# Performance work log

Hardware: AMD Instinct MI355X
Metric: run time of the kernel (lower is better)

The kernel has to match this reference:

```python
import jax, jax.numpy as jnp
import numpy as np

NUM_EXPERTS = 8
TOP_K = 2
INIT_STD = 0.02


def setup_inputs() -> dict:
    key = jax.random.key(0)
    ks = jax.random.split(key, 10)
    B, S, H, I, SI, E = 2, 512, 2048, 1408, 5632, NUM_EXPERTS
    return {
        "hidden_states": jax.random.normal(ks[0], (B, S, H), jnp.float32),
        "gate_w": jax.random.normal(ks[1], (H, E), jnp.float32) * INIT_STD,
        "w_gate": jax.random.normal(ks[2], (E, H, I), jnp.float32) * INIT_STD,
        "w_up": jax.random.normal(ks[3], (E, H, I), jnp.float32) * INIT_STD,
        "w_down": jax.random.normal(ks[4], (E, I, H), jnp.float32) * INIT_STD,
        "sw_gate": jax.random.normal(ks[5], (H, SI), jnp.float32) * INIT_STD,
        "sw_up": jax.random.normal(ks[6], (H, SI), jnp.float32) * INIT_STD,
        "sw_down": jax.random.normal(ks[7], (SI, H), jnp.float32) * INIT_STD,
        "shared_gate_w": jax.random.normal(ks[8], (H, 1), jnp.float32) * INIT_STD,
    }


def reference(hidden_states, gate_w, w_gate, w_up, w_down, sw_gate, sw_up, sw_down, shared_gate_w):
    # Router: logits [B,S,E] in float32, softmax, top-k (norm_topk_prob=False)
    router_logits = (hidden_states @ gate_w).astype(jnp.float32)
    routing_weights = jax.nn.softmax(router_logits, axis=-1)
    top_w, sel = jax.lax.top_k(routing_weights, TOP_K)  # [B,S,K]
    # Scatter top-k weights back to dense per-expert weights [B,S,E]
    # (equals sum_k (sel==e) * top_w, as in the original masked accumulation)
    w = (jax.nn.one_hot(sel, NUM_EXPERTS, dtype=top_w.dtype) * top_w[..., None]).sum(axis=-2)
    # Dense loop over all experts, vectorized as batched einsum (same math)
    g = jnp.einsum('bsh,ehi->bsei', hidden_states, w_gate)
    u = jnp.einsum('bsh,ehi->bsei', hidden_states, w_up)
    expert_out = jnp.einsum('bsei,eih->bseh', jax.nn.silu(g) * u, w_down)  # [B,S,E,H]
    moe_out = jnp.einsum('bse,bseh->bsh', w.astype(hidden_states.dtype), expert_out)
    # Shared expert with sigmoid gate
    shared = (jax.nn.silu(hidden_states @ sw_gate) * (hidden_states @ sw_up)) @ sw_down
    shared = jax.nn.sigmoid(hidden_states @ shared_gate_w) * shared
    return moe_out + shared, router_logits
```

## Files before the change

kernel.cpp:

```cpp
#include <hip/hip_runtime.h>
#include <hip/hip_bf16.h>

#define T_TOK 1024
#define HDIM  2048
#define NEXP  8
#define IDIM  1408
#define SIDIM 5632
#define MAXSLOTS 24

typedef __attribute__((ext_vector_type(8))) short bf16x8;
typedef __attribute__((ext_vector_type(4))) float f32x4;
typedef unsigned short ushort_t;

__device__ __forceinline__ unsigned f2bf(float x) {
    unsigned u = __float_as_uint(x);
    return (u + 0x7fffu + ((u >> 16) & 1u)) >> 16;
}
__device__ __forceinline__ unsigned pack2(float a, float b) {
    return f2bf(a) | (f2bf(b) << 16);
}
__device__ __forceinline__ void async16(const void* g, void* l) {
    __builtin_amdgcn_global_load_lds(
        (const __attribute__((address_space(1))) void*)g,
        (__attribute__((address_space(3))) void*)l, 16, 0, 0);
}

#define PIPE_BAR()    __builtin_amdgcn_s_barrier()
#define SCHED_FENCE() __builtin_amdgcn_sched_barrier(0)
#define WAIT_VM8()    asm volatile("s_waitcnt vmcnt(8)" ::: "memory")
#define WAIT_VM0()    asm volatile("s_waitcnt vmcnt(0)" ::: "memory")

__global__ __launch_bounds__(256) void conv_x(
    const float* __restrict__ src, ushort_t* __restrict__ dst)
{
    const int i = blockIdx.x * 256 + threadIdx.x;
    const float4* s = (const float4*)src + (size_t)i * 2;
    float4 a = s[0], b = s[1];
    union { ushort_t us[8]; uint4 v; } o;
    o.us[0] = (ushort_t)f2bf(a.x); o.us[1] = (ushort_t)f2bf(a.y);
    o.us[2] = (ushort_t)f2bf(a.z); o.us[3] = (ushort_t)f2bf(a.w);
    o.us[4] = (ushort_t)f2bf(b.x); o.us[5] = (ushort_t)f2bf(b.y);
    o.us[6] = (ushort_t)f2bf(b.z); o.us[7] = (ushort_t)f2bf(b.w);
    ((uint4*)dst)[i] = o.v;
}

__global__ __launch_bounds__(256) void conv_all(
    const float* __restrict__ wg, const float* __restrict__ wu,
    const float* __restrict__ wd, const float* __restrict__ swg,
    const float* __restrict__ swu, const float* __restrict__ swd,
    ushort_t* __restrict__ wtg, ushort_t* __restrict__ wtu,
    ushort_t* __restrict__ wtd, ushort_t* __restrict__ swtg,
    ushort_t* __restrict__ swtu, ushort_t* __restrict__ swtd)
{
    int id = blockIdx.x;
    const float* src; ushort_t* dst; int K, N, ktile, ntile;
    if (id < 11264) {
        const float* s0; ushort_t* d0;
        if (id < 5632) { s0 = wg; d0 = wtg; } else { s0 = wu; d0 = wtu; id -= 5632; }
        const int e = id / 704, t = id % 704;
        K = 2048; N = 1408;
        src = s0 + (size_t)e * K * N; dst = d0 + (size_t)e * K * N;
        ntile = t % 22; ktile = t / 22;
    } else if (id < 16896) {
        const int t2 = id - 11264;
        const int e = t2 / 704, t = t2 % 704;
        K = 1408; N = 2048;
        src = wd + (size_t)e * K * N; dst = wtd + (size_t)e * K * N;
        ntile = t % 32; ktile = t / 32;
    } else if (id < 22528) {
        int t2 = id - 16896; const float* s0; ushort_t* d0;
        if (t2 < 2816) { s0 = swg; d0 = swtg; } else { s0 = swu; d0 = swtu; t2 -= 2816; }
        K = 2048; N = 5632;
        src = s0; dst = d0;
        ntile = t2 % 88; ktile = t2 / 88;
    } else {
        const int t2 = id - 22528;
        K = 5632; N = 2048; src = swd; dst = swtd;
        ntile = t2 % 32; ktile = t2 / 32;
    }
    const int tid = threadIdx.x;
    __shared__ __align__(16) unsigned ldsw[32 * 68];
    const float* sp = src + (size_t)(ktile * 64) * N + ntile * 64;
    const int m = tid & 15;
    const int ph = tid >> 4;
#pragma unroll
    for (int h = 0; h < 2; ++h) {
        const int P = ph + h * 16;
        const float* r0 = sp + (size_t)(2 * P) * N + m * 4;
        f32x4 a = __builtin_nontemporal_load((const f32x4*)r0);
        f32x4 b = __builtin_nontemporal_load((const f32x4*)(r0 + N));
        uint4 u;
        u.x = pack2(a[0], b[0]); u.y = pack2(a[1], b[1]);
        u.z = pack2(a[2], b[2]); u.w = pack2(a[3], b[3]);
        *(uint4*)&ldsw[P * 68 + 4 * (m ^ (P >> 2))] = u;
    }
    __syncthreads();
    ushort_t* dp = dst + (size_t)(ntile * 64) * K + ktile * 64;
#pragma unroll
    for (int j = 0; j < 2; ++j) {
        const int c = tid + j * 256;
        const int row = c >> 3, kc = c & 7;
        const int base = 4 * ((row >> 2) ^ kc) + (row & 3);
        uint4 v;
        v.x = ldsw[(4 * kc + 0) * 68 + base];
        v.y = ldsw[(4 * kc + 1) * 68 + base];
        v.z = ldsw[(4 * kc + 2) * 68 + base];
        v.w = ldsw[(4 * kc + 3) * 68 + base];
        *(uint4*)(dp + (size_t)row * K + kc * 8) = v;
    }
}

__global__ __launch_bounds__(256) void router_kernel(
    const float* __restrict__ hs, const float* __restrict__ gw,
    const float* __restrict__ sgw, float* __restrict__ out_logits,
    float* __restrict__ w_dense, float* __restrict__ sgate,
    int* __restrict__ counts, int* __restrict__ tok_list)
{
    const int t = blockIdx.x;
    const int tid = threadIdx.x;
    const float* h = hs + (size_t)t * HDIM;
    float acc[9];
#pragma unroll
    for (int e = 0; e < 9; ++e) acc[e] = 0.f;
    for (int i = tid; i < HDIM; i += 256) {
        float hv = h[i];
        const float4* g4 = (const float4*)(gw + (size_t)i * NEXP);
        float4 g0 = g4[0], g1 = g4[1];
        acc[0] += hv * g0.x; acc[1] += hv * g0.y;
        acc[2] += hv * g0.z; acc[3] += hv * g0.w;
        acc[4] += hv * g1.x; acc[5] += hv * g1.y;
        acc[6] += hv * g1.z; acc[7] += hv * g1.w;
        acc[8] += hv * sgw[i];
    }
#pragma unroll
    for (int e = 0; e < 9; ++e)
        for (int off = 32; off > 0; off >>= 1)
            acc[e] += __shfl_down(acc[e], off, 64);
    __shared__ float lds[4][9];
    const int wid = tid >> 6, lane = tid & 63;
    if (lane == 0)
        for (int e = 0; e < 9; ++e) lds[wid][e] = acc[e];
    __syncthreads();
    if (tid == 0) {
        float l[9];
        for (int e = 0; e < 9; ++e)
            l[e] = lds[0][e] + lds[1][e] + lds[2][e] + lds[3][e];
        for (int e = 0; e < NEXP; ++e) out_logits[(size_t)t * NEXP + e] = l[e];
        float m = l[0];
        for (int e = 1; e < NEXP; ++e) m = fmaxf(m, l[e]);
        float p[NEXP], s = 0.f;
        for (int e = 0; e < NEXP; ++e) { p[e] = expf(l[e] - m); s += p[e]; }
        float inv = 1.f / s;
        for (int e = 0; e < NEXP; ++e) p[e] *= inv;
        int e0 = 0;
        for (int e = 1; e < NEXP; ++e) if (p[e] > p[e0]) e0 = e;
        int e1 = (e0 == 0) ? 1 : 0;
        for (int e = 0; e < NEXP; ++e) if (e != e0 && p[e] > p[e1]) e1 = e;
        for (int e = 0; e < NEXP; ++e)
            w_dense[(size_t)t * NEXP + e] = (e == e0) ? p[e0] : ((e == e1) ? p[e1] : 0.f);
        sgate[t] = 1.f / (1.f + expf(-l[8]));
        int p0 = atomicAdd(&counts[e0], 1); tok_list[e0 * T_TOK + p0] = t;
        int p1 = atomicAdd(&counts[e1], 1); tok_list[e1 * T_TOK + p1] = t;
    }
}

__global__ __launch_bounds__(64) void slot_kernel(
    const int* __restrict__ counts, int* __restrict__ slot_e,
    int* __restrict__ slot_rb, int* __restrict__ nslots)
{
    if (threadIdx.x == 0 && blockIdx.x == 0) {
        int ns = 0;
        for (int e = 0; e < NEXP; ++e)
            for (int b = 0; b < counts[e]; b += 128) {
                slot_e[ns] = e; slot_rb[ns] = b; ++ns;
            }
        nslots[0] = ns;
    }
}

__global__ __launch_bounds__(256) void gateup_all(
    const ushort_t* __restrict__ Xb,
    const ushort_t* __restrict__ swtg, const ushort_t* __restrict__ swtu,
    const ushort_t* __restrict__ wtg, const ushort_t* __restrict__ wtu,
    ushort_t* __restrict__ Ysh, ushort_t* __restrict__ Yr,
    const int* __restrict__ slot_e, const int* __restrict__ slot_rb,
    const int* __restrict__ counts, const int* __restrict__ nslots,
    const int* __restrict__ tok_list, const ushort_t* __restrict__ zerobuf)
{
    const int id = blockIdx.x;
    int n0, slot, e, rowbase, N, mode;
    if (id < 704) {
        mode = 1; n0 = (id % 88) * 64; slot = id / 88; e = 0; rowbase = 0; N = SIDIM;
    } else {
        mode = 0;
        const int id2 = id - 704;
        n0 = (id2 % 22) * 64; slot = id2 / 22;
        if (slot >= nslots[0]) return;
        e = slot_e[slot]; rowbase = slot_rb[slot]; N = IDIM;
    }
    const ushort_t* __restrict__ Wg = mode ? swtg : wtg + (size_t)e * HDIM * IDIM;
    const ushort_t* __restrict__ Wu = mode ? swtu : wtu + (size_t)e * HDIM * IDIM;
    ushort_t* __restrict__ Y = mode ? Ysh : Yr;
    const int K = HDIM;

    const int tid = threadIdx.x, lane = tid & 63, wid = tid >> 6;
    const int wr = (wid >> 1) * 64;
    const int wc = (wid & 1) * 32;
    const int fm = lane & 15, kg = lane >> 4;

    __shared__ int ltok[128];
    __shared__ __align__(16) ushort_t Xa[2][128 * 64];
    __shared__ __align__(16) ushort_t Bgs[2][64 * 64];
    __shared__ __align__(16) ushort_t Bus[2][64 * 64];

    if (tid < 128) {
        int tg;
        if (mode == 0) {
            int cnt = counts[e];
            tg = (rowbase + tid < cnt) ? tok_list[e * T_TOK + rowbase + tid] : -1;
        } else {
            tg = slot * 128 + tid;
        }
        ltok[tid] = tg;
    }
    __syncthreads();

    f32x4 ag[4][2], au[4][2];
#pragma unroll
    for (int a = 0; a < 4; ++a)
#pragma unroll
        for (int b = 0; b < 2; ++b) {
            ag[a][b] = f32x4{0.f, 0.f, 0.f, 0.f};
            au[a][b] = f32x4{0.f, 0.f, 0.f, 0.f};
        }

    const int koff = (((tid & 7) ^ ((tid >> 3) & 7))) * 8;
    const ushort_t* pA[4];
#pragma unroll
    for (int j = 0; j < 4; ++j) {
        const int r = (tid >> 3) + j * 32;
        const int tk = ltok[r];
        pA[j] = (tk >= 0) ? Xb + (size_t)tk * K + koff : zerobuf;
    }
    const ushort_t* pG[2];
    const ushort_t* pU[2];
#pragma unroll
    for (int j = 0; j < 2; ++j) {
        const int r = (tid >> 3) + j * 32;
        pG[j] = Wg + (size_t)(n0 + r) * K + koff;
        pU[j] = Wu + (size_t)(n0 + r) * K + koff;
    }

#define GU_STAGE(xp, gp, up, k0)                                            \
    {                                                                       \
        _Pragma("unroll")                                                   \
        for (int j = 0; j < 4; ++j)                                         \
            async16(pA[j] + (k0), &(xp)[(j * 256 + wid * 64) * 8]);         \
        _Pragma("unroll")                                                   \
        for (int j = 0; j < 2; ++j) {                                       \
            async16(pG[j] + (k0), &(gp)[(j * 256 + wid * 64) * 8]);         \
            async16(pU[j] + (k0), &(up)[(j * 256 + wid * 64) * 8]);         \
        }                                                                   \
    }

#define GU_COMP(xa, bg, bu)                                                 \
    {                                                                       \
        _Pragma("unroll")                                                   \
        for (int ks = 0; ks < 2; ++ks) {                                    \
            const int kx = ((ks * 4 + kg) ^ (fm & 7)) * 8;                  \
            bf16x8 af[4];                                                   \
            _Pragma("unroll")                                               \
            for (int mt = 0; mt < 4; ++mt)                                  \
                af[mt] = *(const bf16x8*)&(xa)[(wr + mt * 16 + fm) * 64 + kx]; \
            _Pragma("unroll")                                               \
            for (int nt = 0; nt < 2; ++nt) {                                \
                const int rb = (wc + nt * 16 + fm) * 64 + kx;               \
                bf16x8 bgv = *(const bf16x8*)&(bg)[rb];                     \
                bf16x8 buv = *(const bf16x8*)&(bu)[rb];                     \
                _Pragma("unroll")                                           \
                for (int mt = 0; mt < 4; ++mt) {                            \
                    ag[mt][nt] = __builtin_amdgcn_mfma_f32_16x16x32_bf16(af[mt], bgv, ag[mt][nt], 0, 0, 0); \
                    au[mt][nt] = __builtin_amdgcn_mfma_f32_16x16x32_bf16(af[mt], buv, au[mt][nt], 0, 0, 0); \
                }                                                           \
            }                                                               \
        }                                                                   \
    }

    const int NT = K / 64;
    GU_STAGE(Xa[0], Bgs[0], Bus[0], 0);
    GU_STAGE(Xa[1], Bgs[1], Bus[1], 64);

    int t = 0;
    for (; t + 3 < NT; t += 2) {
        WAIT_VM8(); PIPE_BAR(); SCHED_FENCE();
        GU_COMP(Xa[0], Bgs[0], Bus[0]);
        SCHED_FENCE(); PIPE_BAR(); SCHED_FENCE();
        GU_STAGE(Xa[0], Bgs[0], Bus[0], (t + 2) * 64);

        WAIT_VM8(); PIPE_BAR(); SCHED_FENCE();
        GU_COMP(Xa[1], Bgs[1], Bus[1]);
        SCHED_FENCE(); PIPE_BAR(); SCHED_FENCE();
        GU_STAGE(Xa[1], Bgs[1], Bus[1], (t + 3) * 64);
    }
    if (t + 2 < NT) {
        WAIT_VM8(); PIPE_BAR(); SCHED_FENCE();
        GU_COMP(Xa[0], Bgs[0], Bus[0]);
        SCHED_FENCE(); PIPE_BAR(); SCHED_FENCE();
        GU_STAGE(Xa[0], Bgs[0], Bus[0], (t + 2) * 64);
        WAIT_VM8(); PIPE_BAR(); SCHED_FENCE();
        GU_COMP(Xa[1], Bgs[1], Bus[1]);
        WAIT_VM0(); PIPE_BAR(); SCHED_FENCE();
        GU_COMP(Xa[0], Bgs[0], Bus[0]);
    } else {
        WAIT_VM8(); PIPE_BAR(); SCHED_FENCE();
        GU_COMP(Xa[0], Bgs[0], Bus[0]);
        WAIT_VM0(); PIPE_BAR(); SCHED_FENCE();
        GU_COMP(Xa[1], Bgs[1], Bus[1]);
    }
#undef GU_STAGE
#undef GU_COMP

#pragma unroll
    for (int mt = 0; mt < 4; ++mt)
#pragma unroll
        for (int nt = 0; nt < 2; ++nt) {
            const int col = n0 + wc + nt * 16 + fm;
#pragma unroll
            for (int i = 0; i < 4; ++i) {
                const int row = wr + mt * 16 + kg * 4 + i;
                float g = ag[mt][nt][i], u = au[mt][nt][i];
                float yv = g / (1.f + expf(-g)) * u;
                Y[(size_t)(slot * 128 + row) * N + col] = (ushort_t)f2bf(yv);
            }
        }
}

__global__ __launch_bounds__(256) void down_all(
    const ushort_t* __restrict__ Ysh, const ushort_t* __restrict__ Yr,
    const ushort_t* __restrict__ swtd, const ushort_t* __restrict__ wtd,
    float* __restrict__ out,
    const int* __restrict__ slot_e, const int* __restrict__ slot_rb,
    const int* __restrict__ counts, const int* __restrict__ nslots,
    const int* __restrict__ tok_list, const float* __restrict__ w_dense,
    const float* __restrict__ sgate)
{
    const int id = blockIdx.x;
    int n0, slot, e, rowbase, K, kbase, ksteps, mode;
    const ushort_t* Yb;
    const ushort_t* Wd;
    if (id < 512) {
        mode = 1;
        n0 = (id & 15) * 128; slot = (id >> 4) & 7;
        const int z = id >> 7;
        K = SIDIM; kbase = z * 1408; ksteps = 22;
        e = 0; rowbase = 0;
        Yb = Ysh + (size_t)slot * 128 * K;
        Wd = swtd;
    } else {
        mode = 0;
        const int id2 = id - 512;
        n0 = (id2 & 15) * 128;
        const int rest = id2 >> 4;
        slot = rest >> 1;
        if (slot >= nslots[0]) return;
        const int z = rest & 1;
        K = IDIM; kbase = z * 704; ksteps = 11;
        e = slot_e[slot]; rowbase = slot_rb[slot];
        Yb = Yr + (size_t)slot * 128 * K;
        Wd = wtd + (size_t)e * IDIM * HDIM;
    }
    const int tid = threadIdx.x, lane = tid & 63, wid = tid >> 6;
    const int wr = (wid >> 1) * 64;
    const int wc = (wid & 1) * 64;
    const int fm = lane & 15, kg = lane >> 4;

    __shared__ int ltok[128];
    __shared__ float lw[128];
    __shared__ __align__(16) ushort_t Ya[2][128 * 64];
    __shared__ __align__(16) ushort_t Bd[2][128 * 64];

    if (tid < 128) {
        int tg; float wv;
        if (mode == 0) {
            int cnt = counts[e];
            if (rowbase + tid < cnt) {
                tg = tok_list[e * T_TOK + rowbase + tid];
                wv = w_dense[(size_t)tg * NEXP + e];
            } else { tg = -1; wv = 0.f; }
        } else {
            tg = slot * 128 + tid; wv = sgate[tg];
        }
        ltok[tid] = tg; lw[tid] = wv;
    }
    __syncthreads();

    f32x4 acc[4][4];
#pragma unroll
    for (int a = 0; a < 4; ++a)
#pragma unroll
        for (int b = 0; b < 4; ++b) acc[a][b] = f32x4{0.f, 0.f, 0.f, 0.f};

    const int koff = (((tid & 7) ^ ((tid >> 3) & 7))) * 8;
    const ushort_t* pY[4];
    const ushort_t* pW[4];
#pragma unroll
    for (int j = 0; j < 4; ++j) {
        const int r = (tid >> 3) + j * 32;
        pY[j] = Yb + (size_t)r * K + kbase + koff;
        pW[j] = Wd + (size_t)(n0 + r) * K + kbase + koff;
    }

#define D_STAGE(yp, bp, k0)                                                 \
    {                                                                       \
        _Pragma("unroll")                                                   \
        for (int j = 0; j < 4; ++j) {                                       \
            async16(pY[j] + (k0), &(yp)[(j * 256 + wid * 64) * 8]);         \
            async16(pW[j] + (k0), &(bp)[(j * 256 + wid * 64) * 8]);         \
        }                                                                   \
    }

#define D_COMP(ya, bd)                                                      \
    {                                                                       \
        _Pragma("unroll")                                                   \
        for (int ks = 0; ks < 2; ++ks) {                                    \
            const int kx = ((ks * 4 + kg) ^ (fm & 7)) * 8;                  \
            bf16x8 af[4];                                                   \
            _Pragma("unroll")                                               \
            for (int mt = 0; mt < 4; ++mt)                                  \
                af[mt] = *(const bf16x8*)&(ya)[(wr + mt * 16 + fm) * 64 + kx]; \
            _Pragma("unroll")                                               \
            for (int nt = 0; nt < 4; ++nt) {                                \
                bf16x8 bfv = *(const bf16x8*)&(bd)[(wc + nt * 16 + fm) * 64 + kx]; \
                _Pragma("unroll")                                           \
                for (int mt = 0; mt < 4; ++mt)                              \
                    acc[mt][nt] = __builtin_amdgcn_mfma_f32_16x16x32_bf16(af[mt], bfv, acc[mt][nt], 0, 0, 0); \
            }                                                               \
        }                                                                   \
    }

    const int NT = ksteps;
    D_STAGE(Ya[0], Bd[0], 0);
    D_STAGE(Ya[1], Bd[1], 64);

    int t = 0;
    for (; t + 3 < NT; t += 2) {
        WAIT_VM8(); PIPE_BAR(); SCHED_FENCE();
        D_COMP(Ya[0], Bd[0]);
        SCHED_FENCE(); PIPE_BAR(); SCHED_FENCE();
        D_STAGE(Ya[0], Bd[0], (t + 2) * 64);

        WAIT_VM8(); PIPE_BAR(); SCHED_FENCE();
        D_COMP(Ya[1], Bd[1]);
        SCHED_FENCE(); PIPE_BAR(); SCHED_FENCE();
        D_STAGE(Ya[1], Bd[1], (t + 3) * 64);
    }
    if (t + 2 < NT) {
        WAIT_VM8(); PIPE_BAR(); SCHED_FENCE();
        D_COMP(Ya[0], Bd[0]);
        SCHED_FENCE(); PIPE_BAR(); SCHED_FENCE();
        D_STAGE(Ya[0], Bd[0], (t + 2) * 64);
        WAIT_VM8(); PIPE_BAR(); SCHED_FENCE();
        D_COMP(Ya[1], Bd[1]);
        WAIT_VM0(); PIPE_BAR(); SCHED_FENCE();
        D_COMP(Ya[0], Bd[0]);
    } else {
        WAIT_VM8(); PIPE_BAR(); SCHED_FENCE();
        D_COMP(Ya[0], Bd[0]);
        WAIT_VM0(); PIPE_BAR(); SCHED_FENCE();
        D_COMP(Ya[1], Bd[1]);
    }
#undef D_STAGE
#undef D_COMP

#pragma unroll
    for (int mt = 0; mt < 4; ++mt)
#pragma unroll
        for (int nt = 0; nt < 4; ++nt) {
            const int col = n0 + wc + nt * 16 + fm;
#pragma unroll
            for (int i = 0; i < 4; ++i) {
                const int row = wr + mt * 16 + kg * 4 + i;
                const int tg = ltok[row];
                if (tg >= 0)
                    atomicAdd(out + (size_t)tg * HDIM + col, lw[row] * acc[mt][nt][i]);
            }
        }
}

extern "C" void kernel_launch(void* const* d_in, const int* in_sizes, int n_in,
                              void* d_out, int out_size, void* d_ws, size_t ws_size,
                              hipStream_t stream)
{
    const float* hs  = (const float*)d_in[0];
    const float* gw  = (const float*)d_in[1];
    const float* wg  = (const float*)d_in[2];
    const float* wu  = (const float*)d_in[3];
    const float* wd  = (const float*)d_in[4];
    const float* swg = (const float*)d_in[5];
    const float* swu = (const float*)d_in[6];
    const float* swd = (const float*)d_in[7];
    const float* sgw = (const float*)d_in[8];
    float* out = (float*)d_out;
    char* ws = (char*)d_ws;

    float* w_dense      = (float*)(ws + 0x00000);
    float* sgate        = (float*)(ws + 0x08000);
    int* counts         = (int*)(ws + 0x09000);
    int* nslots         = (int*)(ws + 0x09100);
    int* slot_e         = (int*)(ws + 0x09200);
    int* slot_rb        = (int*)(ws + 0x09300);
    int* tok_list       = (int*)(ws + 0x09400);
    ushort_t* zerobuf   = (ushort_t*)(ws + 0x11400);
    ushort_t* Xb        = (ushort_t*)(ws + 0x20000);
    ushort_t* Yr        = (ushort_t*)(ws + 0x420000);
    ushort_t* Ysh       = (ushort_t*)(ws + 0xC60000);
    ushort_t* wtg       = (ushort_t*)(ws + 0x1760000);
    ushort_t* wtu       = (ushort_t*)(ws + 0x4360000);
    ushort_t* wtd       = (ushort_t*)(ws + 0x6F60000);
    ushort_t* swtg      = (ushort_t*)(ws + 0x9B60000);
    ushort_t* swtu      = (ushort_t*)(ws + 0xB160000);
    ushort_t* swtd      = (ushort_t*)(ws + 0xC760000);
    float* out_logits = out + (size_t)T_TOK * HDIM;

    hipMemsetAsync(counts, 0, 256, stream);
    hipMemsetAsync(zerobuf, 0, 16384, stream);
    hipMemsetAsync(out, 0, (size_t)T_TOK * HDIM * sizeof(float), stream);

    conv_x<<<dim3(1024), dim3(256), 0, stream>>>(hs, Xb);
    conv_all<<<dim3(25344), dim3(256), 0, stream>>>(
        wg, wu, wd, swg, swu, swd, wtg, wtu, wtd, swtg, swtu, swtd);

    router_kernel<<<dim3(T_TOK), dim3(256), 0, stream>>>(
        hs, gw, sgw, out_logits, w_dense, sgate, counts, tok_list);
    slot_kernel<<<dim3(1), dim3(64), 0, stream>>>(counts, slot_e, slot_rb, nslots);

    gateup_all<<<dim3(704 + 22 * MAXSLOTS), dim3(256), 0, stream>>>(
        Xb, swtg, swtu, wtg, wtu, Ysh, Yr,
        slot_e, slot_rb, counts, nslots, tok_list, zerobuf);

    down_all<<<dim3(512 + 16 * MAXSLOTS * 2), dim3(256), 0, stream>>>(
        Ysh, Yr, swtd, wtd, out,
        slot_e, slot_rb, counts, nslots, tok_list, w_dense, sgate);
}
```

Baseline: 609.9 us.

## Replace atomic scatter in down projection with partial buffers and combine kernel

The down-projection kernel no longer scatters weighted results into the output with float atomics. It writes plain fp32 partial tiles: four K-split planes for the shared expert, and one plane per routed slot with the routed K-split removed. A new combine kernel then sums the shared partials, applies the sigmoid gate and the two routing weights, and gathers the routed rows through positions recorded by the router. This removes the atomic traffic and the output memset, but adds a large partial-buffer write and read plus an extra launch. The double-buffered async pipeline is also replaced with a simpler single-buffer loop with two barriers per step, which loses load/compute overlap.

```diff
diff --git a/kernel.cpp b/kernel.cpp
--- a/kernel.cpp
+++ b/kernel.cpp
@@ -113,7 +113,8 @@
 __global__ __launch_bounds__(256) void router_kernel(
     const float* __restrict__ hs, const float* __restrict__ gw,
     const float* __restrict__ sgw, float* __restrict__ out_logits,
-    float* __restrict__ w_dense, float* __restrict__ sgate,
+    float* __restrict__ aw, int* __restrict__ apos,
+    float* __restrict__ sgate,
     int* __restrict__ counts, int* __restrict__ tok_list)
 {
     const int t = blockIdx.x;
@@ -156,24 +157,29 @@
         for (int e = 1; e < NEXP; ++e) if (p[e] > p[e0]) e0 = e;
         int e1 = (e0 == 0) ? 1 : 0;
         for (int e = 0; e < NEXP; ++e) if (e != e0 && p[e] > p[e1]) e1 = e;
-        for (int e = 0; e < NEXP; ++e)
-            w_dense[(size_t)t * NEXP + e] = (e == e0) ? p[e0] : ((e == e1) ? p[e1] : 0.f);
         sgate[t] = 1.f / (1.f + expf(-l[8]));
         int p0 = atomicAdd(&counts[e0], 1); tok_list[e0 * T_TOK + p0] = t;
         int p1 = atomicAdd(&counts[e1], 1); tok_list[e1 * T_TOK + p1] = t;
+        aw[t * 2]     = p[e0];
+        aw[t * 2 + 1] = p[e1];
+        apos[t * 2]     = (e0 << 10) | p0;
+        apos[t * 2 + 1] = (e1 << 10) | p1;
     }
 }
 
 __global__ __launch_bounds__(64) void slot_kernel(
     const int* __restrict__ counts, int* __restrict__ slot_e,
-    int* __restrict__ slot_rb, int* __restrict__ nslots)
+    int* __restrict__ slot_rb, int* __restrict__ nslots,
+    int* __restrict__ sbase)
 {
     if (threadIdx.x == 0 && blockIdx.x == 0) {
         int ns = 0;
-        for (int e = 0; e < NEXP; ++e)
+        for (int e = 0; e < NEXP; ++e) {
+            sbase[e] = ns;
             for (int b = 0; b < counts[e]; b += 128) {
                 slot_e[ns] = e; slot_rb[ns] = b; ++ns;
             }
+        }
         nslots[0] = ns;
     }
 }
@@ -338,61 +344,39 @@
 __global__ __launch_bounds__(256) void down_all(
     const ushort_t* __restrict__ Ysh, const ushort_t* __restrict__ Yr,
     const ushort_t* __restrict__ swtd, const ushort_t* __restrict__ wtd,
-    float* __restrict__ out,
-    const int* __restrict__ slot_e, const int* __restrict__ slot_rb,
-    const int* __restrict__ counts, const int* __restrict__ nslots,
-    const int* __restrict__ tok_list, const float* __restrict__ w_dense,
-    const float* __restrict__ sgate)
+    float* __restrict__ Psh, float* __restrict__ Prt,
+    const int* __restrict__ slot_e, const int* __restrict__ nslots)
 {
     const int id = blockIdx.x;
-    int n0, slot, e, rowbase, K, kbase, ksteps, mode;
+    int n0, slot, kbase, K;
     const ushort_t* Yb;
     const ushort_t* Wd;
+    float* P;
     if (id < 512) {
-        mode = 1;
         n0 = (id & 15) * 128; slot = (id >> 4) & 7;
         const int z = id >> 7;
-        K = SIDIM; kbase = z * 1408; ksteps = 22;
-        e = 0; rowbase = 0;
+        K = SIDIM; kbase = z * 1408;
         Yb = Ysh + (size_t)slot * 128 * K;
         Wd = swtd;
+        P = Psh + ((size_t)z * T_TOK + (size_t)slot * 128) * HDIM;
     } else {
-        mode = 0;
         const int id2 = id - 512;
         n0 = (id2 & 15) * 128;
-        const int rest = id2 >> 4;
-        slot = rest >> 1;
+        slot = id2 >> 4;
         if (slot >= nslots[0]) return;
-        const int z = rest & 1;
-        K = IDIM; kbase = z * 704; ksteps = 11;
-        e = slot_e[slot]; rowbase = slot_rb[slot];
+        const int e = slot_e[slot];
+        K = IDIM; kbase = 0;
         Yb = Yr + (size_t)slot * 128 * K;
         Wd = wtd + (size_t)e * IDIM * HDIM;
+        P = Prt + (size_t)slot * 128 * HDIM;
     }
     const int tid = threadIdx.x, lane = tid & 63, wid = tid >> 6;
     const int wr = (wid >> 1) * 64;
     const int wc = (wid & 1) * 64;
     const int fm = lane & 15, kg = lane >> 4;
 
-    __shared__ int ltok[128];
-    __shared__ float lw[128];
-    __shared__ __align__(16) ushort_t Ya[2][128 * 64];
-    __shared__ __align__(16) ushort_t Bd[2][128 * 64];
-
-    if (tid < 128) {
-        int tg; float wv;
-        if (mode == 0) {
-            int cnt = counts[e];
-            if (rowbase + tid < cnt) {
-                tg = tok_list[e * T_TOK + rowbase + tid];
-                wv = w_dense[(size_t)tg * NEXP + e];
-            } else { tg = -1; wv = 0.f; }
-        } else {
-            tg = slot * 128 + tid; wv = sgate[tg];
-        }
-        ltok[tid] = tg; lw[tid] = wv;
-    }
-    __syncthreads();
+    __shared__ __align__(16) ushort_t Ya[128 * 64];
+    __shared__ __align__(16) ushort_t Bd[128 * 64];
 
     f32x4 acc[4][4];
 #pragma unroll
@@ -410,67 +394,32 @@
         pW[j] = Wd + (size_t)(n0 + r) * K + kbase + koff;
     }
 
-#define D_STAGE(yp, bp, k0)                                                 \
-    {                                                                       \
-        _Pragma("unroll")                                                   \
-        for (int j = 0; j < 4; ++j) {                                       \
-            async16(pY[j] + (k0), &(yp)[(j * 256 + wid * 64) * 8]);         \
-            async16(pW[j] + (k0), &(bp)[(j * 256 + wid * 64) * 8]);         \
-        }                                                                   \
-    }
-
-#define D_COMP(ya, bd)                                                      \
-    {                                                                       \
-        _Pragma("unroll")                                                   \
-        for (int ks = 0; ks < 2; ++ks) {                                    \
-            const int kx = ((ks * 4 + kg) ^ (fm & 7)) * 8;                  \
-            bf16x8 af[4];                                                   \
-            _Pragma("unroll")                                               \
-            for (int mt = 0; mt < 4; ++mt)                                  \
-                af[mt] = *(const bf16x8*)&(ya)[(wr + mt * 16 + fm) * 64 + kx]; \
-            _Pragma("unroll")                                               \
-            for (int nt = 0; nt < 4; ++nt) {                                \
-                bf16x8 bfv = *(const bf16x8*)&(bd)[(wc + nt * 16 + fm) * 64 + kx]; \
-                _Pragma("unroll")                                           \
-                for (int mt = 0; mt < 4; ++mt)                              \
-                    acc[mt][nt] = __builtin_amdgcn_mfma_f32_16x16x32_bf16(af[mt], bfv, acc[mt][nt], 0, 0, 0); \
-            }                                                               \
-        }                                                                   \
-    }
-
-    const int NT = ksteps;
-    D_STAGE(Ya[0], Bd[0], 0);
-    D_STAGE(Ya[1], Bd[1], 64);
-
-    int t = 0;
-    for (; t + 3 < NT; t += 2) {
-        WAIT_VM8(); PIPE_BAR(); SCHED_FENCE();
-        D_COMP(Ya[0], Bd[0]);
-        SCHED_FENCE(); PIPE_BAR(); SCHED_FENCE();
-        D_STAGE(Ya[0], Bd[0], (t + 2) * 64);
-
-        WAIT_VM8(); PIPE_BAR(); SCHED_FENCE();
-        D_COMP(Ya[1], Bd[1]);
-        SCHED_FENCE(); PIPE_BAR(); SCHED_FENCE();
-        D_STAGE(Ya[1], Bd[1], (t + 3) * 64);
-    }
-    if (t + 2 < NT) {
-        WAIT_VM8(); PIPE_BAR(); SCHED_FENCE();
-        D_COMP(Ya[0], Bd[0]);
-        SCHED_FENCE(); PIPE_BAR(); SCHED_FENCE();
-        D_STAGE(Ya[0], Bd[0], (t + 2) * 64);
-        WAIT_VM8(); PIPE_BAR(); SCHED_FENCE();
-        D_COMP(Ya[1], Bd[1]);
-        WAIT_VM0(); PIPE_BAR(); SCHED_FENCE();
-        D_COMP(Ya[0], Bd[0]);
-    } else {
-        WAIT_VM8(); PIPE_BAR(); SCHED_FENCE();
-        D_COMP(Ya[0], Bd[0]);
-        WAIT_VM0(); PIPE_BAR(); SCHED_FENCE();
-        D_COMP(Ya[1], Bd[1]);
-    }
-#undef D_STAGE
-#undef D_COMP
+    for (int s = 0; s < 22; ++s) {
+        const int k0 = s * 64;
+#pragma unroll
+        for (int j = 0; j < 4; ++j) {
+            async16(pY[j] + k0, &Ya[(j * 256 + wid * 64) * 8]);
+            async16(pW[j] + k0, &Bd[(j * 256 + wid * 64) * 8]);
+        }
+        __syncthreads();
+
+#pragma unroll
+        for (int ks = 0; ks < 2; ++ks) {
+            const int kx = ((ks * 4 + kg) ^ (fm & 7)) * 8;
+            bf16x8 af[4];
+#pragma unroll
+            for (int mt = 0; mt < 4; ++mt)
+                af[mt] = *(const bf16x8*)&Ya[(wr + mt * 16 + fm) * 64 + kx];
+#pragma unroll
+            for (int nt = 0; nt < 4; ++nt) {
+                bf16x8 bfv = *(const bf16x8*)&Bd[(wc + nt * 16 + fm) * 64 + kx];
+#pragma unroll
+                for (int mt = 0; mt < 4; ++mt)
+                    acc[mt][nt] = __builtin_amdgcn_mfma_f32_16x16x32_bf16(af[mt], bfv, acc[mt][nt], 0, 0, 0);
+            }
+        }
+        __syncthreads();
+    }
 
 #pragma unroll
     for (int mt = 0; mt < 4; ++mt)
@@ -480,11 +429,42 @@
 #pragma unroll
             for (int i = 0; i < 4; ++i) {
                 const int row = wr + mt * 16 + kg * 4 + i;
-                const int tg = ltok[row];
-                if (tg >= 0)
-                    atomicAdd(out + (size_t)tg * HDIM + col, lw[row] * acc[mt][nt][i]);
+                P[(size_t)row * HDIM + col] = acc[mt][nt][i];
             }
         }
+}
+
+__global__ __launch_bounds__(256) void combine_kernel(
+    const float* __restrict__ Psh, const float* __restrict__ Prt,
+    const float* __restrict__ sgate, const float* __restrict__ aw,
+    const int* __restrict__ apos, const int* __restrict__ sbase,
+    float* __restrict__ out)
+{
+    const int t = blockIdx.x;
+    const int c = threadIdx.x * 8;
+    const float sg = sgate[t];
+    const float w0 = aw[t * 2], w1 = aw[t * 2 + 1];
+    const int a0 = apos[t * 2], a1 = apos[t * 2 + 1];
+    const size_t r0 = (size_t)(sbase[a0 >> 10] * 128 + (a0 & 1023)) * HDIM + c;
+    const size_t r1 = (size_t)(sbase[a1 >> 10] * 128 + (a1 & 1023)) * HDIM + c;
+    const size_t tc = (size_t)t * HDIM + c;
+    const size_t plane = (size_t)T_TOK * HDIM;
+
+    f32x4 s0 = *(const f32x4*)(Psh + tc);
+    f32x4 s1 = *(const f32x4*)(Psh + tc + 4);
+#pragma unroll
+    for (int z = 1; z < 4; ++z) {
+        s0 += *(const f32x4*)(Psh + z * plane + tc);
+        s1 += *(const f32x4*)(Psh + z * plane + tc + 4);
+    }
+    f32x4 q0 = *(const f32x4*)(Prt + r0);
+    f32x4 q1 = *(const f32x4*)(Prt + r0 + 4);
+    f32x4 u0 = *(const f32x4*)(Prt + r1);
+    f32x4 u1 = *(const f32x4*)(Prt + r1 + 4);
+    f32x4 o0 = sg * s0 + w0 * q0 + w1 * u0;
+    f32x4 o1 = sg * s1 + w0 * q1 + w1 * u1;
+    *(f32x4*)(out + tc) = o0;
+    *(f32x4*)(out + tc + 4) = o1;
 }
 
 extern "C" void kernel_launch(void* const* d_in, const int* in_sizes, int n_in,
@@ -503,14 +483,16 @@
     float* out = (float*)d_out;
     char* ws = (char*)d_ws;
 
-    float* w_dense      = (float*)(ws + 0x00000);
     float* sgate        = (float*)(ws + 0x08000);
     int* counts         = (int*)(ws + 0x09000);
     int* nslots         = (int*)(ws + 0x09100);
     int* slot_e         = (int*)(ws + 0x09200);
     int* slot_rb        = (int*)(ws + 0x09300);
+    int* sbase          = (int*)(ws + 0x09380);
     int* tok_list       = (int*)(ws + 0x09400);
     ushort_t* zerobuf   = (ushort_t*)(ws + 0x11400);
+    float* aw           = (float*)(ws + 0x15400);
+    int* apos           = (int*)(ws + 0x17400);
     ushort_t* Xb        = (ushort_t*)(ws + 0x20000);
     ushort_t* Yr        = (ushort_t*)(ws + 0x420000);
     ushort_t* Ysh       = (ushort_t*)(ws + 0xC60000);
@@ -520,25 +502,28 @@
     ushort_t* swtg      = (ushort_t*)(ws + 0x9B60000);
     ushort_t* swtu      = (ushort_t*)(ws + 0xB160000);
     ushort_t* swtd      = (ushort_t*)(ws + 0xC760000);
+    float* Psh          = (float*)(ws + 0x1760000);
+    float* Prt          = (float*)(ws + 0x3760000);
     float* out_logits = out + (size_t)T_TOK * HDIM;
 
     hipMemsetAsync(counts, 0, 256, stream);
     hipMemsetAsync(zerobuf, 0, 16384, stream);
-    hipMemsetAsync(out, 0, (size_t)T_TOK * HDIM * sizeof(float), stream);
 
     conv_x<<<dim3(1024), dim3(256), 0, stream>>>(hs, Xb);
     conv_all<<<dim3(25344), dim3(256), 0, stream>>>(
         wg, wu, wd, swg, swu, swd, wtg, wtu, wtd, swtg, swtu, swtd);
 
     router_kernel<<<dim3(T_TOK), dim3(256), 0, stream>>>(
-        hs, gw, sgw, out_logits, w_dense, sgate, counts, tok_list);
-    slot_kernel<<<dim3(1), dim3(64), 0, stream>>>(counts, slot_e, slot_rb, nslots);
+        hs, gw, sgw, out_logits, aw, apos, sgate, counts, tok_list);
+    slot_kernel<<<dim3(1), dim3(64), 0, stream>>>(counts, slot_e, slot_rb, nslots, sbase);
 
     gateup_all<<<dim3(704 + 22 * MAXSLOTS), dim3(256), 0, stream>>>(
         Xb, swtg, swtu, wtg, wtu, Ysh, Yr,
         slot_e, slot_rb, counts, nslots, tok_list, zerobuf);
 
-    down_all<<<dim3(512 + 16 * MAXSLOTS * 2), dim3(256), 0, stream>>>(
-        Ysh, Yr, swtd, wtd, out,
-        slot_e, slot_rb, counts, nslots, tok_list, w_dense, sgate);
-}
+    down_all<<<dim3(512 + 16 * MAXSLOTS), dim3(256), 0, stream>>>(
+        Ysh, Yr, swtd, wtd, Psh, Prt, slot_e, nslots);
+
+    combine_kernel<<<dim3(T_TOK), dim3(256), 0, stream>>>(
+        Psh, Prt, sgate, aw, apos, sbase, out);
+}
```

Result: faster. 573.0 us (-6.1%).
